# Performance work log

Measured on AMD Instinct MI355X. Metric: run time of the kernel, lower is better.

## Reference

```python
import jax, jax.numpy as jnp
import numpy as np

N_NODES, N_EDGES, N_GRAPHS = 8192, 32768, 256
FXD, HEADS = 78, 10
D2 = FXD * HEADS  # 780
FF = 2048
L_MUT = 735
NF = 32
OUT_DIM = 128


def _ln(x, g, b, eps=1e-5):
    m = x.mean(-1, keepdims=True)
    v = ((x - m) ** 2).mean(-1, keepdims=True)
    return (x - m) * jax.lax.rsqrt(v + eps) * g + b


def _transformer(x, in_w, in_b, out_w, out_b, ln1_g, ln1_b, l1_w, l1_b, l2_w, l2_b, ln2_g, ln2_b):
    # post-LN TransformerEncoderLayer, nhead=1, seq = all N nodes, batch = 1 (eval: dropout off)
    E = x.shape[-1]
    q, k, v = jnp.split(x @ in_w.T + in_b, 3, axis=-1)
    a = jax.nn.softmax((q @ k.T) * (1.0 / np.sqrt(E)), axis=-1) @ v  # [N,N] scores
    x = _ln(x + a @ out_w.T + out_b, ln1_g, ln1_b)
    h = jax.nn.relu(x @ l1_w.T + l1_b) @ l2_w.T + l2_b
    return _ln(x + h, ln2_g, ln2_b)


def _gat(x, src, dst, w, a_src, a_dst, bias):
    # PyG GATConv, heads=10, concat=True, leaky 0.2, self loops already in src/dst
    N = x.shape[0]
    h = (x @ w.T).reshape(N, HEADS, FXD)
    asrc = (h * a_src).sum(-1)  # [N,H]
    adst = (h * a_dst).sum(-1)
    alpha = jax.nn.leaky_relu(asrc[src] + adst[dst], 0.2)  # [E,H]
    amax = jax.lax.stop_gradient(jax.ops.segment_max(alpha, dst, num_segments=N))
    ex = jnp.exp(alpha - amax[dst])
    coef = ex / (jax.ops.segment_sum(ex, dst, num_segments=N)[dst] + 1e-16)
    out = jax.ops.segment_sum(coef[:, :, None] * h[src], dst, num_segments=N)
    return out.reshape(N, HEADS * FXD) + bias


def _gcn(x, src, dst, w, b):
    # PyG GCNConv with self loops (already in src/dst), symmetric norm
    N = x.shape[0]
    deg = jax.ops.segment_sum(jnp.ones(dst.shape, x.dtype), dst, num_segments=N)
    dis = jnp.where(deg > 0, jax.lax.rsqrt(jnp.maximum(deg, 1.0)), 0.0)
    norm = dis[src] * dis[dst]
    return jax.ops.segment_sum(norm[:, None] * (x @ w.T)[src], dst, num_segments=N) + b


def _conv1d(x, w, b):
    y = jax.lax.conv_general_dilated(x, w, (1,), 'VALID', dimension_numbers=('NCH', 'OIH', 'NCH'))
    return y + b[None, :, None]


def _convT1d(x, w, b):
    # torch ConvTranspose1d weight [in,out,k] -> flipped [out,in,k], full padding
    k = w.shape[-1]
    ker = jnp.flip(w, -1).transpose(1, 0, 2)
    y = jax.lax.conv_general_dilated(x, ker, (1,), [(k - 1, k - 1)], dimension_numbers=('NCH', 'OIH', 'NCH'))
    return y + b[None, :, None]


def _maxpool1d(x, k):
    return jax.lax.reduce_window(x, -jnp.inf, jax.lax.max, (1, 1, k), (1, 1, k), 'VALID')


def _bn_eval(x, g, b, eps=1e-5):
    # eval-mode BatchNorm1d with fresh running stats (mean 0, var 1)
    return x * (g / np.sqrt(1.0 + eps))[None, :, None] + b[None, :, None]


def _forward(edge_index, batch, x, target_mut, t1_in_w, t1_in_b, t1_out_w, t1_out_b, t1_ln1_g, t1_ln1_b, t1_l1_w, t1_l1_b, t1_l2_w, t1_l2_b, t1_ln2_g, t1_ln2_b, gat_w, gat_asrc, gat_adst, gat_b, t2_in_w, t2_in_b, t2_out_w, t2_out_b, t2_ln1_g, t2_ln1_b, t2_l1_w, t2_l1_b, t2_l2_w, t2_l2_b, t2_ln2_g, t2_ln2_b, gcn_w, gcn_b, fcg1_w, fcg1_b, fcg2_w, fcg2_b, e1_w, e1_b, bn1_g, bn1_b, e2_w, e2_b, bn2_g, bn2_b, e3_w, e3_b, enc_lin_w, enc_lin_b, d3_w, d3_b, dbn2_g, dbn2_b, d2_w, d2_b, dbn1_g, dbn1_b, d1_w, d1_b, fc1_w, fc1_b, fc2_w, fc2_b, out_w, out_b):
    N = x.shape[0]
    xg = _transformer(x, t1_in_w, t1_in_b, t1_out_w, t1_out_b, t1_ln1_g, t1_ln1_b, t1_l1_w, t1_l1_b, t1_l2_w, t1_l2_b, t1_ln2_g, t1_ln2_b)
    loops = jnp.arange(N, dtype=edge_index.dtype)
    src = jnp.concatenate([edge_index[0], loops])
    dst = jnp.concatenate([edge_index[1], loops])
    xg = jax.nn.relu(_gat(xg, src, dst, gat_w, gat_asrc, gat_adst, gat_b))
    xg = _transformer(xg, t2_in_w, t2_in_b, t2_out_w, t2_out_b, t2_ln1_g, t2_ln1_b, t2_l1_w, t2_l1_b, t2_l2_w, t2_l2_b, t2_ln2_g, t2_ln2_b)
    xg = jax.nn.relu(_gcn(xg, src, dst, gcn_w, gcn_b))
    gm = jax.ops.segment_max(xg, batch, num_segments=N_GRAPHS)
    gm = jnp.where(jnp.isfinite(gm), gm, 0.0)
    cnt = jax.ops.segment_sum(jnp.ones((N,), xg.dtype), batch, num_segments=N_GRAPHS)
    ga = jax.ops.segment_sum(xg, batch, num_segments=N_GRAPHS) / jnp.maximum(cnt, 1.0)[:, None]
    xd = jnp.concatenate([gm, ga], axis=1)  # [B, 1560]
    xd = jax.nn.relu(xd @ fcg1_w.T + fcg1_b)
    xd = xd @ fcg2_w.T + fcg2_b  # [B, 128]
    # conv1d autoencoder on mutation profile
    t = target_mut[:, None, :]  # [B,1,735]
    e = jax.nn.leaky_relu(_bn_eval(_maxpool1d(_conv1d(t, e1_w, e1_b), 8), bn1_g, bn1_b))
    e = jax.nn.leaky_relu(_bn_eval(_maxpool1d(_conv1d(e, e2_w, e2_b), 7), bn2_g, bn2_b))
    e = _conv1d(e, e3_w, e3_b)  # [B,128,5]
    z = e.reshape(e.shape[0], -1) @ enc_lin_w.T + enc_lin_b  # [B,128]
    d = jnp.repeat(jax.nn.leaky_relu(_bn_eval(_convT1d(e, d3_w, d3_b), dbn2_g, dbn2_b)), 7, axis=-1)
    d = jnp.repeat(jax.nn.leaky_relu(_bn_eval(_convT1d(d, d2_w, d2_b), dbn1_g, dbn1_b)), 8, axis=-1)
    decode = _convT1d(d, d1_w, d1_b)  # [B,1,735]
    xc = jnp.concatenate([xd, z], axis=1)
    xc = jax.nn.relu(xc @ fc1_w.T + fc1_b)
    xc = jax.nn.relu(xc @ fc2_w.T + fc2_b)
    out = jax.nn.sigmoid(xc @ out_w.T + out_b)
    return (out, xd, decode)


def setup_inputs():
    key = jax.random.key(0)
    ks = iter(jax.random.split(key, 64))

    def rn(*shape):
        return jax.random.normal(next(ks), shape, jnp.float32) * 0.05

    inp = {}
    inp['x'] = jax.random.normal(next(ks), (N_NODES, FXD), jnp.float32)
    inp['edge_index'] = jax.random.randint(next(ks), (2, N_EDGES), 0, N_NODES)
    inp['batch'] = jnp.sort(jax.random.randint(next(ks), (N_NODES,), 0, N_GRAPHS))
    inp['target_mut'] = jax.random.normal(next(ks), (N_GRAPHS, L_MUT), jnp.float32)
    for p, E in (('t1', FXD), ('t2', D2)):
        inp[p + '_in_w'] = rn(3 * E, E); inp[p + '_in_b'] = jnp.zeros((3 * E,))
        inp[p + '_out_w'] = rn(E, E); inp[p + '_out_b'] = jnp.zeros((E,))
        inp[p + '_ln1_g'] = jnp.ones((E,)); inp[p + '_ln1_b'] = jnp.zeros((E,))
        inp[p + '_l1_w'] = rn(FF, E); inp[p + '_l1_b'] = jnp.zeros((FF,))
        inp[p + '_l2_w'] = rn(E, FF); inp[p + '_l2_b'] = jnp.zeros((E,))
        inp[p + '_ln2_g'] = jnp.ones((E,)); inp[p + '_ln2_b'] = jnp.zeros((E,))
    inp['gat_w'] = rn(D2, FXD); inp['gat_asrc'] = rn(HEADS, FXD); inp['gat_adst'] = rn(HEADS, FXD); inp['gat_b'] = jnp.zeros((D2,))
    inp['gcn_w'] = rn(D2, D2); inp['gcn_b'] = jnp.zeros((D2,))
    inp['fcg1_w'] = rn(1500, 2 * D2); inp['fcg1_b'] = jnp.zeros((1500,))
    inp['fcg2_w'] = rn(OUT_DIM, 1500); inp['fcg2_b'] = jnp.zeros((OUT_DIM,))
    inp['e1_w'] = rn(NF, 1, 8); inp['e1_b'] = jnp.zeros((NF,))
    inp['bn1_g'] = jnp.ones((NF,)); inp['bn1_b'] = jnp.zeros((NF,))
    inp['e2_w'] = rn(2 * NF, NF, 8); inp['e2_b'] = jnp.zeros((2 * NF,))
    inp['bn2_g'] = jnp.ones((2 * NF,)); inp['bn2_b'] = jnp.zeros((2 * NF,))
    inp['e3_w'] = rn(4 * NF, 2 * NF, 8); inp['e3_b'] = jnp.zeros((4 * NF,))
    inp['enc_lin_w'] = rn(OUT_DIM, 640); inp['enc_lin_b'] = jnp.zeros((OUT_DIM,))
    inp['d3_w'] = rn(4 * NF, 2 * NF, 8); inp['d3_b'] = jnp.zeros((2 * NF,))
    inp['dbn2_g'] = jnp.ones((2 * NF,)); inp['dbn2_b'] = jnp.zeros((2 * NF,))
    inp['d2_w'] = rn(2 * NF, NF, 8); inp['d2_b'] = jnp.zeros((NF,))
    inp['dbn1_g'] = jnp.ones((NF,)); inp['dbn1_b'] = jnp.zeros((NF,))
    inp['d1_w'] = rn(NF, 1, 8); inp['d1_b'] = jnp.zeros((1,))
    inp['fc1_w'] = rn(1024, 2 * OUT_DIM); inp['fc1_b'] = jnp.zeros((1024,))
    inp['fc2_w'] = rn(128, 1024); inp['fc2_b'] = jnp.zeros((128,))
    inp['out_w'] = rn(1, 128); inp['out_b'] = jnp.zeros((1,))
    return inp


def reference(x, edge_index, batch, target_mut, t1_in_w, t1_in_b, t1_out_w, t1_out_b, t1_ln1_g, t1_ln1_b, t1_l1_w, t1_l1_b, t1_l2_w, t1_l2_b, t1_ln2_g, t1_ln2_b, gat_w, gat_asrc, gat_adst, gat_b, t2_in_w, t2_in_b, t2_out_w, t2_out_b, t2_ln1_g, t2_ln1_b, t2_l1_w, t2_l1_b, t2_l2_w, t2_l2_b, t2_ln2_g, t2_ln2_b, gcn_w, gcn_b, fcg1_w, fcg1_b, fcg2_w, fcg2_b, e1_w, e1_b, bn1_g, bn1_b, e2_w, e2_b, bn2_g, bn2_b, e3_w, e3_b, enc_lin_w, enc_lin_b, d3_w, d3_b, dbn2_g, dbn2_b, d2_w, d2_b, dbn1_g, dbn1_b, d1_w, d1_b, fc1_w, fc1_b, fc2_w, fc2_b, out_w, out_b):
    return _forward(edge_index, batch, x, target_mut, t1_in_w, t1_in_b, t1_out_w, t1_out_b, t1_ln1_g, t1_ln1_b, t1_l1_w, t1_l1_b, t1_l2_w, t1_l2_b, t1_ln2_g, t1_ln2_b, gat_w, gat_asrc, gat_adst, gat_b, t2_in_w, t2_in_b, t2_out_w, t2_out_b, t2_ln1_g, t2_ln1_b, t2_l1_w, t2_l1_b, t2_l2_w, t2_l2_b, t2_ln2_g, t2_ln2_b, gcn_w, gcn_b, fcg1_w, fcg1_b, fcg2_w, fcg2_b, e1_w, e1_b, bn1_g, bn1_b, e2_w, e2_b, bn2_g, bn2_b, e3_w, e3_b, enc_lin_w, enc_lin_b, d3_w, d3_b, dbn2_g, dbn2_b, d2_w, d2_b, dbn1_g, dbn1_b, d1_w, d1_b, fc1_w, fc1_b, fc2_w, fc2_b, out_w, out_b)
```

## Files before the change

### kernel.cpp

```cpp
#include <hip/hip_runtime.h>
#include <math.h>

#define NN     8192
#define NEDGE  32768
#define NETOT  40960
#define NG     256
#define FXD_   78
#define NH     10
#define DD2    780
#define FFD    2048
#define LMUT   735

static inline int cdiv_i(long long a, int b){ return (int)((a + (long long)b - 1) / b); }
static inline int pad32(int x){ return (x + 31) & ~31; }

typedef __attribute__((ext_vector_type(8))) short bf16x8;
typedef __attribute__((ext_vector_type(4))) float f32x4;

static __device__ __forceinline__ unsigned short f2bf(float f){
    unsigned u = __float_as_uint(f);
    u += 0x7FFFu + ((u >> 16) & 1u);
    return (unsigned short)(u >> 16);
}

static __device__ __forceinline__ void gload16(const void* g, void* l){
    __builtin_amdgcn_global_load_lds((const __attribute__((address_space(1))) void*)g,
                                     (__attribute__((address_space(3))) void*)l, 16, 0, 0);
}

__global__ void fill_f32_k(float* __restrict__ p, float v, long long n){
    long long i = (long long)blockIdx.x * 256 + threadIdx.x;
    if (i < n) p[i] = v;
}
__global__ void fill_u32_k(unsigned* __restrict__ p, unsigned v, long long n){
    long long i = (long long)blockIdx.x * 256 + threadIdx.x;
    if (i < n) p[i] = v;
}

__global__ void cvt_pad_k(const float* __restrict__ src, unsigned short* __restrict__ dst,
                          long long n , int C, int lds_, int ldd)
{
    long long i = (long long)blockIdx.x * 256 + threadIdx.x;
    if (i >= n) return;
    int r = (int)(i / ldd), c = (int)(i % ldd);
    dst[i] = (c < C) ? f2bf(src[(size_t)r * lds_ + c]) : (unsigned short)0;
}

__global__ void tr_bf16_k(const unsigned short* __restrict__ src, unsigned short* __restrict__ dst,
                          int R, int C, int lds_, int ldd)
{
    __shared__ unsigned short t[32][33];
    int cb = blockIdx.x * 32, rb = blockIdx.y * 32;
    int tx = threadIdx.x & 31, ty = threadIdx.x >> 5;
#pragma unroll
    for (int i = 0; i < 4; ++i){
        int r = rb + ty + i * 8, c = cb + tx;
        t[ty + i * 8][tx] = (r < R && c < C) ? src[(size_t)r * lds_ + c] : (unsigned short)0;
    }
    __syncthreads();
#pragma unroll
    for (int i = 0; i < 4; ++i){
        int dr = cb + ty + i * 8, dc = rb + tx;
        if (dr < C && dc < R) dst[(size_t)dr * ldd + dc] = t[tx][ty + i * 8];
    }
}

__global__ void qkv_bias_k(const float* __restrict__ b3, float* __restrict__ out, int E, int Ep)
{
    int idx = blockIdx.x * 256 + threadIdx.x;
    if (idx >= 3 * Ep) return;
    int s = idx / Ep, c = idx % Ep;
    out[idx] = (c < E) ? b3[s * E + c] : 0.f;
}

__global__ void bias_add_k(float* __restrict__ X, const float* __restrict__ b, long long n, int cols)
{
    long long i = (long long)blockIdx.x * 256 + threadIdx.x;
    if (i < n) X[i] += b[i % cols];
}

template<int OUTC, int ACT, int SPLITK, int BROW, int BN>
__global__ __launch_bounds__(256) void mgemm_k(
    const unsigned short* __restrict__ A, const unsigned short* __restrict__ B,
    const float* __restrict__ bias, void* __restrict__ Cv,
    int M, int N, int Kp, int lda, int ldb, int ldc, int swz)
{
    constexpr int NFJ   = BN / 32;
    constexpr int TILEA = 128 * 32;
    constexpr int TILEB = BN * 32;
    __shared__ unsigned short As[2 * TILEA];
    __shared__ unsigned short Bs[2 * TILEB];
    const int tid = threadIdx.x;
    const int lane = tid & 63, wid = tid >> 6;
    const int r16 = lane & 15, q = lane >> 4;
    const int wr = (wid >> 1) * 64, wc = (wid & 1) * (BN / 2);

    const int gx = gridDim.x, gy = gridDim.y;
    const int nwg = gx * gy;
    int orig = swz ? ((int)blockIdx.x * gy + (int)blockIdx.y)
                   : ((int)blockIdx.y * gx + (int)blockIdx.x);
    int q8 = nwg >> 3, r8 = nwg & 7;
    int xcd = orig & 7, kk8 = orig >> 3;
    int wgid = (xcd < r8 ? xcd * (q8 + 1) : r8 * (q8 + 1) + (xcd - r8) * q8) + kk8;
    int bx, by;
    if (swz){ by = wgid % gy; bx = wgid / gy; }
    else    { bx = wgid % gx; by = wgid / gx; }
    const int row0 = by * 128, col0 = bx * BN;

    int kbeg = 0, kend = Kp;
    if (SPLITK > 1){
        int nt_ = Kp >> 5, cpt = (nt_ + SPLITK - 1) / SPLITK;
        kbeg = (int)blockIdx.z * cpt * 32;
        kend = min(Kp, kbeg + cpt * 32);
    }

    const int c0 = wid * 128 + lane;
    const int r0a = c0 >> 2, k0a = (c0 & 3) << 3;
    const size_t gA0 = (size_t)min(row0 + r0a, M - 1) * lda + k0a;
    const size_t gA1 = (size_t)min(row0 + r0a + 16, M - 1) * lda + k0a;
    unsigned short* lA = As + wid * 1024;
    size_t gB0 = 0, gB1 = 0;
    unsigned short* lB;
    if (BN == 128){
        gB0 = (size_t)min(col0 + r0a, N - 1) * ldb + k0a;
        gB1 = (size_t)min(col0 + r0a + 16, N - 1) * ldb + k0a;
        lB = Bs + wid * 1024;
    } else {
        const int cb = wid * 64 + lane;
        const int rb_ = cb >> 2, kb_ = (cb & 3) << 3;
        gB0 = (size_t)min(col0 + rb_, N - 1) * ldb + kb_;
        lB = Bs + wid * 512;
    }

    f32x4 acc[4][NFJ];
#pragma unroll
    for (int i = 0; i < 4; ++i)
#pragma unroll
        for (int j = 0; j < NFJ; ++j){ f32x4 z = {0.f, 0.f, 0.f, 0.f}; acc[i][j] = z; }

    const int nt = (kend - kbeg) >> 5;
    if (nt > 0){
        gload16(A + gA0 + kbeg, lA);
        gload16(A + gA1 + kbeg, lA + 512);
        gload16(B + gB0 + kbeg, lB);
        if (BN == 128) gload16(B + gB1 + kbeg, lB + 512);
        __syncthreads();
        int cur = 0;
        for (int t = 0; t < nt; ++t){
            const int k0 = kbeg + (t << 5);
            if (t + 1 < nt){
                const int kn = k0 + 32, nb = cur ^ 1;
                gload16(A + gA0 + kn, lA + nb * TILEA);
                gload16(A + gA1 + kn, lA + nb * TILEA + 512);
                gload16(B + gB0 + kn, lB + nb * TILEB);
                if (BN == 128) gload16(B + gB1 + kn, lB + nb * TILEB + 512);
            }
            const unsigned short* Ab = As + cur * TILEA;
            const unsigned short* Bb = Bs + cur * TILEB;
            bf16x8 af[4], bfv[NFJ];
#pragma unroll
            for (int f = 0; f < 4; ++f)
                af[f] = *(const bf16x8*)(Ab + (size_t)(wr + f * 16 + r16) * 32 + (q << 3));
#pragma unroll
            for (int f = 0; f < NFJ; ++f)
                bfv[f] = *(const bf16x8*)(Bb + (size_t)(wc + f * 16 + r16) * 32 + (q << 3));
#pragma unroll
            for (int fi = 0; fi < 4; ++fi)
#pragma unroll
                for (int fj = 0; fj < NFJ; ++fj)
                    acc[fi][fj] = __builtin_amdgcn_mfma_f32_16x16x32_bf16(af[fi], bfv[fj], acc[fi][fj], 0, 0, 0);
            __syncthreads();
            cur ^= 1;
        }
    }

#pragma unroll
    for (int fi = 0; fi < 4; ++fi){
#pragma unroll
        for (int j = 0; j < 4; ++j){
            int r = row0 + wr + fi * 16 + q * 4 + j;
            if (r >= M) continue;
#pragma unroll
            for (int fj = 0; fj < NFJ; ++fj){
                int c = col0 + wc + fj * 16 + r16;
                if (c >= N) continue;
                float v = acc[fi][fj][j];
                if (SPLITK > 1){
                    atomicAdd((float*)Cv + (size_t)r * ldc + c, v);
                } else {
                    if (bias) v += BROW ? bias[r] : bias[c];
                    if (ACT == 1) v = fmaxf(v, 0.f);
                    if (ACT == 2) v = 1.f / (1.f + expf(-v));
                    if (OUTC == 0) ((float*)Cv)[(size_t)r * ldc + c] = v;
                    else ((unsigned short*)Cv)[(size_t)r * ldc + c] = f2bf(v);
                }
            }
        }
    }
}

template<int OUTC, int ACT, int SPLITK, int BROW, int BN>
static void mgemm(hipStream_t s, const unsigned short* A, const unsigned short* B,
                  const float* bias, void* C, int M, int N, int Kp,
                  int lda, int ldb, int ldc, int swz)
{
    dim3 g(cdiv_i(N, BN), cdiv_i(M, 128), SPLITK);
    mgemm_k<OUTC, ACT, SPLITK, BROW, BN><<<g, 256, 0, s>>>(A, B, bias, C, M, N, Kp, lda, ldb, ldc, swz);
}

__global__ __launch_bounds__(256) void softmax_bf16_k(unsigned short* __restrict__ SP, float scale)
{
    __shared__ float red[8];
    const int tid = threadIdx.x;
    uint4* prow = (uint4*)(SP + (size_t)blockIdx.x * NN);
    float v[32];
    float mx = -3.4e38f;
#pragma unroll
    for (int c = 0; c < 4; ++c){
        uint4 t = prow[c * 256 + tid];
        const unsigned* u = (const unsigned*)&t;
#pragma unroll
        for (int j = 0; j < 4; ++j){
            float lo = __uint_as_float(u[j] << 16) * scale;
            float hi = __uint_as_float(u[j] & 0xFFFF0000u) * scale;
            v[c * 8 + j * 2]     = lo;
            v[c * 8 + j * 2 + 1] = hi;
            mx = fmaxf(mx, fmaxf(lo, hi));
        }
    }
#pragma unroll
    for (int off = 32; off; off >>= 1) mx = fmaxf(mx, __shfl_xor(mx, off, 64));
    if ((tid & 63) == 0) red[tid >> 6] = mx;
    __syncthreads();
    mx = fmaxf(fmaxf(red[0], red[1]), fmaxf(red[2], red[3]));
    float sum = 0.f;
#pragma unroll
    for (int i = 0; i < 32; ++i){ v[i] = expf(v[i] - mx); sum += v[i]; }
#pragma unroll
    for (int off = 32; off; off >>= 1) sum += __shfl_xor(sum, off, 64);
    if ((tid & 63) == 0) red[4 + (tid >> 6)] = sum;
    __syncthreads();
    float inv = 1.f / (red[4] + red[5] + red[6] + red[7]);
#pragma unroll
    for (int c = 0; c < 4; ++c){
        uint4 t;
        unsigned* u = (unsigned*)&t;
#pragma unroll
        for (int j = 0; j < 4; ++j){
            unsigned lo = f2bf(v[c * 8 + j * 2] * inv);
            unsigned hi = f2bf(v[c * 8 + j * 2 + 1] * inv);
            u[j] = lo | (hi << 16);
        }
        prow[c * 256 + tid] = t;
    }
}

__global__ __launch_bounds__(256) void add_ln_k(
    const float* __restrict__ X, const float* __restrict__ Y, const float* __restrict__ ybias,
    const float* __restrict__ g, const float* __restrict__ b,
    float* __restrict__ out, unsigned short* __restrict__ obf, int E, int Ep)
{
    __shared__ float s1[256], s2[256];
    const int tid = threadIdx.x;
    long long base = (long long)blockIdx.x * E;
    float vals[4];
    float sum = 0.f, sq = 0.f;
    int i = 0;
    for (int c = tid; c < Ep; c += 256, ++i){
        float v = 0.f;
        if (c < E){
            v = X[base + c] + Y[base + c];
            if (ybias) v += ybias[c];
            sum += v; sq += v * v;
        }
        vals[i] = v;
    }
    s1[tid] = sum; s2[tid] = sq; __syncthreads();
    for (int s = 128; s; s >>= 1){
        if (tid < s){ s1[tid] += s1[tid + s]; s2[tid] += s2[tid + s]; }
        __syncthreads();
    }
    float mean = s1[0] / (float)E;
    float var = s2[0] / (float)E - mean * mean;
    if (var < 0.f) var = 0.f;
    float inv = 1.f / sqrtf(var + 1e-5f);
    i = 0;
    for (int c = tid; c < Ep; c += 256, ++i){
        if (c < E){
            float o = (vals[i] - mean) * inv * g[c] + b[c];
            out[base + c] = o;
            if (obf) obf[(size_t)blockIdx.x * Ep + c] = f2bf(o);
        } else if (obf) obf[(size_t)blockIdx.x * Ep + c] = 0;
    }
}

static __device__ __forceinline__ unsigned enc_f(float x){
    unsigned u = __float_as_uint(x);
    return (u & 0x80000000u) ? ~u : (u | 0x80000000u);
}
static __device__ __forceinline__ float dec_f(unsigned u){
    return (u & 0x80000000u) ? __uint_as_float(u & 0x7fffffffu) : __uint_as_float(~u);
}
static __device__ __forceinline__ void edge_sd(const int* __restrict__ ei, int e, int& s, int& d){
    if (e < NEDGE){ s = ei[e]; d = ei[NEDGE + e]; }
    else { s = e - NEDGE; d = e - NEDGE; }
}

__global__ void gat_srcdst_k(const float* __restrict__ h, const float* __restrict__ aw_src,
                             const float* __restrict__ aw_dst, float* __restrict__ asrc,
                             float* __restrict__ adst)
{
    int idx = blockIdx.x * 256 + threadIdx.x;
    if (idx >= NN * NH) return;
    int n = idx / NH, hh = idx % NH;
    const float* hp = h + (long long)n * DD2 + hh * FXD_;
    const float* ws = aw_src + hh * FXD_;
    const float* wd = aw_dst + hh * FXD_;
    float s1 = 0.f, s2 = 0.f;
    for (int f = 0; f < FXD_; ++f){ float v = hp[f]; s1 += v * ws[f]; s2 += v * wd[f]; }
    asrc[idx] = s1; adst[idx] = s2;
}

__global__ void gat_alpha_k(const int* __restrict__ ei, const float* __restrict__ asrc,
                            const float* __restrict__ adst, float* __restrict__ alpha,
                            unsigned* __restrict__ amax)
{
    int idx = blockIdx.x * 256 + threadIdx.x;
    if (idx >= NETOT * NH) return;
    int e = idx / NH, hh = idx % NH;
    int s, d; edge_sd(ei, e, s, d);
    float a = asrc[s * NH + hh] + adst[d * NH + hh];
    a = (a > 0.f) ? a : 0.2f * a;
    alpha[idx] = a;
    atomicMax(&amax[d * NH + hh], enc_f(a));
}

__global__ void gat_expsum_k(const int* __restrict__ ei, float* __restrict__ alpha,
                             const unsigned* __restrict__ amax, float* __restrict__ denom)
{
    int idx = blockIdx.x * 256 + threadIdx.x;
    if (idx >= NETOT * NH) return;
    int e = idx / NH, hh = idx % NH;
    int s, d; edge_sd(ei, e, s, d);
    float m = dec_f(amax[d * NH + hh]);
    float ex = expf(alpha[idx] - m);
    alpha[idx] = ex;
    atomicAdd(&denom[d * NH + hh], ex);
}

__global__ void deg_count_k(const int* __restrict__ ei, int* __restrict__ deg)
{
    int e = blockIdx.x * 256 + threadIdx.x;
    if (e >= NETOT) return;
    int s, d; edge_sd(ei, e, s, d);
    atomicAdd(&deg[d], 1);
}

__global__ __launch_bounds__(256) void csr_off_k(const int* __restrict__ deg,
                                                 int* __restrict__ off, int* __restrict__ cur)
{
    __shared__ int pref[257];
    const int tid = threadIdx.x;
    int loc[32];
    int base = tid * 32, sum = 0;
#pragma unroll
    for (int i = 0; i < 32; ++i){ loc[i] = sum; sum += deg[base + i]; }
    __shared__ int part[256];
    part[tid] = sum; __syncthreads();
    if (tid == 0){
        pref[0] = 0;
        for (int i = 0; i < 256; ++i) pref[i + 1] = pref[i] + part[i];
    }
    __syncthreads();
    int p0 = pref[tid];
#pragma unroll
    for (int i = 0; i < 32; ++i){ off[base + i] = p0 + loc[i]; cur[base + i] = p0 + loc[i]; }
    if (tid == 0) off[NN] = pref[256];
}

__global__ void csr_fill_k(const int* __restrict__ ei, int* __restrict__ cur,
                           int* __restrict__ csr_s, int* __restrict__ csr_e)
{
    int e = blockIdx.x * 256 + threadIdx.x;
    if (e >= NETOT) return;
    int s, d; edge_sd(ei, e, s, d);
    int pos = atomicAdd(&cur[d], 1);
    csr_s[pos] = s; csr_e[pos] = e;
}

__global__ __launch_bounds__(256) void gat_gather_k(
    const int* __restrict__ off, const int* __restrict__ csr_s, const int* __restrict__ csr_e,
    const float* __restrict__ ex, const float* __restrict__ denom,
    const float* __restrict__ hfeat, float* __restrict__ out)
{
    const int d = blockIdx.x, tid = threadIdx.x;
    const int beg = off[d], end = off[d + 1];
    for (int f = tid; f < DD2; f += 256){
        int hh = f / FXD_;
        float acc = 0.f;
        for (int p = beg; p < end; ++p)
            acc += ex[csr_e[p] * NH + hh] * hfeat[(size_t)csr_s[p] * DD2 + f];
        out[(size_t)d * DD2 + f] = acc / (denom[d * NH + hh] + 1e-16f);
    }
}

__global__ __launch_bounds__(256) void gcn_gather_k(
    const int* __restrict__ off, const int* __restrict__ csr_s,
    const float* __restrict__ dis, const float* __restrict__ xw, float* __restrict__ out)
{
    const int d = blockIdx.x, tid = threadIdx.x;
    const int beg = off[d], end = off[d + 1];
    const float dd_ = dis[d];
    for (int f = tid; f < DD2; f += 256){
        float acc = 0.f;
        for (int p = beg; p < end; ++p){
            int s = csr_s[p];
            acc += dis[s] * xw[(size_t)s * DD2 + f];
        }
        out[(size_t)d * DD2 + f] = acc * dd_;
    }
}

__global__ void bias_relu_k(float* __restrict__ X, const float* __restrict__ b,
                            unsigned short* __restrict__ obf, int rows, int cols, int ldp)
{
    long long i = (long long)blockIdx.x * 256 + threadIdx.x;
    if (i >= (long long)rows * ldp) return;
    int r = (int)(i / ldp), c = (int)(i % ldp);
    if (c < cols){
        float v = X[(size_t)r * cols + c] + b[c];
        v = v > 0.f ? v : 0.f;
        X[(size_t)r * cols + c] = v;
        if (obf) obf[i] = f2bf(v);
    } else if (obf) obf[i] = 0;
}

__global__ void dis_k(const int* __restrict__ deg, float* __restrict__ dis)
{
    int n = blockIdx.x * 256 + threadIdx.x;
    if (n >= NN) return;
    float d = (float)deg[n];
    dis[n] = (d > 0.f) ? 1.f / sqrtf(fmaxf(d, 1.f)) : 0.f;
}

__global__ void pool_accum_k(const float* __restrict__ xg, const int* __restrict__ batch,
                             float* __restrict__ gm, float* __restrict__ ga, int* __restrict__ cnt)
{
    long long idx = (long long)blockIdx.x * 256 + threadIdx.x;
    if (idx >= (long long)NN * DD2) return;
    int n = (int)(idx / DD2), f = (int)(idx % DD2);
    int g = batch[n];
    float v = xg[idx];
    atomicMax((int*)(gm + (long long)g * DD2 + f), __float_as_int(v));
    atomicAdd(ga + (long long)g * DD2 + f, v);
    if (f == 0) atomicAdd(cnt + g, 1);
}

__global__ void pool_fin_k(const float* __restrict__ gm, const float* __restrict__ ga,
                           const int* __restrict__ cnt, unsigned short* __restrict__ xdb)
{
    int idx = blockIdx.x * 256 + threadIdx.x;
    if (idx >= NG * 1568) return;
    int g = idx / 1568, c = idx % 1568;
    float v = 0.f;
    if (c < DD2)       v = gm[g * DD2 + c];
    else if (c < 1560) v = ga[g * DD2 + (c - DD2)] / fmaxf((float)cnt[g], 1.f);
    xdb[idx] = f2bf(v);
}

#define BN_SCALE 0.9999950000374996f

__global__ __launch_bounds__(256) void enc1_b(const float* __restrict__ tm, const float* __restrict__ w,
                                              const float* __restrict__ bias, const float* __restrict__ bng,
                                              const float* __restrict__ bnb, float* __restrict__ out)
{
    __shared__ float xs[736];
    __shared__ float ws[256], bs[32], gs[32], b2[32];
    const int g = blockIdx.x, tid = threadIdx.x;
    for (int i = tid; i < 735; i += 256) xs[i] = tm[(size_t)g * LMUT + i];
    ws[tid] = w[tid];
    if (tid < 32){ bs[tid] = bias[tid]; gs[tid] = bng[tid]; b2[tid] = bnb[tid]; }
    __syncthreads();
    for (int idx = tid; idx < 32 * 91; idx += 256){
        int o = idx / 91, t = idx % 91;
        float mx = -3.4e38f;
        for (int p = 0; p < 8; ++p){
            float s = bs[o];
#pragma unroll
            for (int k = 0; k < 8; ++k) s += xs[t * 8 + p + k] * ws[o * 8 + k];
            mx = fmaxf(mx, s);
        }
        float v = mx * gs[o] * BN_SCALE + b2[o];
        out[(size_t)g * 2912 + idx] = v > 0.f ? v : 0.01f * v;
    }
}

__global__ void i2c_enc2_k(const float* __restrict__ in, unsigned short* __restrict__ A){
    int idx = blockIdx.x * 256 + threadIdx.x;
    if (idx >= NG * 84 * 256) return;
    int col = idx & 255, row = idx >> 8;
    int g = row / 84, u = row % 84;
    int i = col >> 3, k = col & 7;
    A[idx] = f2bf(in[(size_t)g * 2912 + i * 91 + u + k]);
}
__global__ void post_enc2_k(const float* __restrict__ G, const float* __restrict__ b,
                            const float* __restrict__ bng, const float* __restrict__ bnb,
                            float* __restrict__ out){
    int idx = blockIdx.x * 256 + threadIdx.x;
    if (idx >= NG * 768) return;
    int t = idx % 12, o = (idx / 12) & 63, g = idx / 768;
    float mx = -3.4e38f;
#pragma unroll
    for (int p = 0; p < 7; ++p) mx = fmaxf(mx, G[(size_t)(g * 84 + t * 7 + p) * 64 + o]);
    float v = (mx + b[o]) * bng[o] * BN_SCALE + bnb[o];
    out[(size_t)g * 768 + o * 12 + t] = v > 0.f ? v : 0.01f * v;
}
__global__ void i2c_enc3_k(const float* __restrict__ in, unsigned short* __restrict__ A){
    int idx = blockIdx.x * 256 + threadIdx.x;
    if (idx >= NG * 5 * 512) return;
    int col = idx & 511, row = idx >> 9;
    int g = row / 5, t = row % 5;
    int i2 = col >> 3, k = col & 7;
    A[idx] = f2bf(in[(size_t)g * 768 + i2 * 12 + t + k]);
}
__global__ void post_enc3_k(const float* __restrict__ G, const float* __restrict__ b,
                            float* __restrict__ e3o, unsigned short* __restrict__ obf){
    int idx = blockIdx.x * 256 + threadIdx.x;
    if (idx >= NG * 640) return;
    int t = idx % 5, o = (idx / 5) & 127, g = idx / 640;
    float v = G[(size_t)(g * 5 + t) * 128 + o] + b[o];
    e3o[(size_t)g * 640 + o * 5 + t] = v;
    obf[(size_t)g * 640 + o * 5 + t] = f2bf(v);
}
__global__ void wshuf_k(const float* __restrict__ src, unsigned short* __restrict__ dst, int I, int O){
    int idx = blockIdx.x * 256 + threadIdx.x;
    if (idx >= I * O * 8) return;
    int o = idx / (I * 8), rem = idx % (I * 8);
    int i = rem >> 3, j = rem & 7;
    dst[idx] = f2bf(src[(size_t)(i * O + o) * 8 + j]);
}
__global__ void i2c_dec3_k(const float* __restrict__ e3o, unsigned short* __restrict__ A){
    int idx = blockIdx.x * 256 + threadIdx.x;
    if (idx >= NG * 12 * 1024) return;
    int col = idx & 1023, row = idx >> 10;
    int g = row / 12, t = row % 12;
    int i2 = col >> 3, j = col & 7;
    int tt = t - j;
    A[idx] = (tt >= 0 && tt < 5) ? f2bf(e3o[(size_t)g * 640 + i2 * 5 + tt]) : (unsigned short)0;
}
__global__ void post_dec3_k(const float* __restrict__ G, const float* __restrict__ b,
                            const float* __restrict__ bng, const float* __restrict__ bnb,
                            float* __restrict__ dd3){
    int idx = blockIdx.x * 256 + threadIdx.x;
    if (idx >= NG * 768) return;
    int t = idx % 12, o = (idx / 12) & 63, g = idx / 768;
    float v = (G[(size_t)(g * 12 + t) * 64 + o] + b[o]) * bng[o] * BN_SCALE + bnb[o];
    dd3[(size_t)g * 768 + o * 12 + t] = v > 0.f ? v : 0.01f * v;
}
__global__ void i2c_dec2_k(const float* __restrict__ dd3, unsigned short* __restrict__ A){
    int idx = blockIdx.x * 256 + threadIdx.x;
    if (idx >= NG * 91 * 512) return;
    int col = idx & 511, row = idx >> 9;
    int g = row / 91, t = row % 91;
    int i2 = col >> 3, j = col & 7;
    int tt = t - j;
    A[idx] = (tt >= 0 && tt < 84) ? f2bf(dd3[(size_t)g * 768 + i2 * 12 + tt / 7]) : (unsigned short)0;
}
__global__ void post_dec2_k(const float* __restrict__ G, const float* __restrict__ b,
                            const float* __restrict__ bng, const float* __restrict__ bnb,
                            float* __restrict__ dd2){
    int idx = blockIdx.x * 256 + threadIdx.x;
    if (idx >= NG * 2912) return;
    int t = idx % 91, o = (idx / 91) & 31, g = idx / 2912;
    float v = (G[(size_t)(g * 91 + t) * 32 + o] + b[o]) * bng[o] * BN_SCALE + bnb[o];
    dd2[(size_t)g * 2912 + o * 91 + t] = v > 0.f ? v : 0.01f * v;
}

__global__ __launch_bounds__(256) void dec1_b(const float* __restrict__ dd2, const float* __restrict__ w,
                                              const float* __restrict__ bias, float* __restrict__ out)
{
    __shared__ float d2s[32][91];
    __shared__ float ws[256];
    const int g = blockIdx.x, tid = threadIdx.x;
    const int t0 = (int)blockIdx.y * 245;
    for (int i = tid; i < 32 * 91; i += 256) d2s[i / 91][i % 91] = dd2[(size_t)g * 2912 + i];
    ws[tid] = w[tid];
    __syncthreads();
    if (tid < 245){
        int t = t0 + tid;
        int id8[8]; bool ok[8];
#pragma unroll
        for (int j = 0; j < 8; ++j){
            int tt = t - j;
            ok[j] = (tt >= 0 && tt < 728);
            id8[j] = ok[j] ? (tt >> 3) : 0;
        }
        float s = bias[0];
        for (int i2 = 0; i2 < 32; ++i2){
            const float* wp = ws + i2 * 8;
            float a = 0.f;
#pragma unroll
            for (int j = 0; j < 8; ++j) if (ok[j]) a += d2s[i2][id8[j]] * wp[j];
            s += a;
        }
        out[(size_t)g * 735 + t] = s;
    }
}

__global__ void concat_xc_k(const float* __restrict__ xd, const float* __restrict__ z,
                            unsigned short* __restrict__ xcb)
{
    int idx = blockIdx.x * 256 + threadIdx.x;
    if (idx >= NG * 256) return;
    int g = idx >> 8, c = idx & 255;
    xcb[idx] = f2bf((c < 128) ? xd[g * 128 + c] : z[g * 128 + (c - 128)]);
}

extern "C" void kernel_launch(void* const* d_in, const int* in_sizes, int n_in,
                              void* d_out, int out_size, void* d_ws, size_t ws_size,
                              hipStream_t stream)
{
    (void)in_sizes; (void)n_in; (void)out_size;

    const float* x      = (const float*)d_in[0];
    const int*   ei     = (const int*)  d_in[1];
    const int*   batch  = (const int*)  d_in[2];
    const float* tmut   = (const float*)d_in[3];
    const float* t1w[12]; for (int i = 0; i < 12; ++i) t1w[i] = (const float*)d_in[4 + i];
    const float* t2w[12]; for (int i = 0; i < 12; ++i) t2w[i] = (const float*)d_in[16 + i];
    const float* gat_w    = (const float*)d_in[28];
    const float* gat_asrc = (const float*)d_in[29];
    const float* gat_adst = (const float*)d_in[30];
    const float* gat_b    = (const float*)d_in[31];
    const float* gcn_w  = (const float*)d_in[32];
    const float* gcn_b  = (const float*)d_in[33];
    const float* fcg1_w = (const float*)d_in[34];
    const float* fcg1_b = (const float*)d_in[35];
    const float* fcg2_w = (const float*)d_in[36];
    const float* fcg2_b = (const float*)d_in[37];
    const float* e1_w = (const float*)d_in[38]; const float* e1_b = (const float*)d_in[39];
    const float* bn1_g = (const float*)d_in[40]; const float* bn1_b = (const float*)d_in[41];
    const float* e2_w = (const float*)d_in[42]; const float* e2_b = (const float*)d_in[43];
    const float* bn2_g = (const float*)d_in[44]; const float* bn2_b = (const float*)d_in[45];
    const float* e3_w = (const float*)d_in[46]; const float* e3_b = (const float*)d_in[47];
    const float* enc_w = (const float*)d_in[48]; const float* enc_b = (const float*)d_in[49];
    const float* d3_w = (const float*)d_in[50]; const float* d3_b = (const float*)d_in[51];
    const float* dbn2_g = (const float*)d_in[52]; const float* dbn2_b = (const float*)d_in[53];
    const float* d2_w = (const float*)d_in[54]; const float* d2_b = (const float*)d_in[55];
    const float* dbn1_g = (const float*)d_in[56]; const float* dbn1_b = (const float*)d_in[57];
    const float* d1_w = (const float*)d_in[58]; const float* d1_b = (const float*)d_in[59];
    const float* fc1_w = (const float*)d_in[60]; const float* fc1_b = (const float*)d_in[61];
    const float* fc2_w = (const float*)d_in[62]; const float* fc2_b = (const float*)d_in[63];
    const float* outw = (const float*)d_in[64]; const float* outb = (const float*)d_in[65];

    float *A1, *A2, *A3, *A4, *X1f, *QBIASf;
    unsigned short *XB, *QKVb, *Vt, *HbPb;
    unsigned short *WQKVb, *WOUTb, *WL1b, *WL2b, *WGb, *WGCNb, *WFCG1b, *WFCG2b,
                   *WENCb, *WFC1b, *WFC2b, *WOUTWb, *XD16, *FG1b, *E3b, *XCb, *FH1b, *FH2b, *Wcvb;
    float *asrc, *adst, *alpha, *denom, *dis, *gm, *ga, *c1p, *c2p, *e3o,
          *zz, *dd3, *dd2b;
    unsigned *amax; int *deg, *cnt, *csr_off, *csr_cur, *csr_s, *csr_e;

    auto carve = [&](long long RB) -> size_t {
        char* wp_ = (char*)d_ws;
        auto alc = [&](size_t bytes) -> char* {
            char* p = wp_;
            wp_ += (bytes + 255) & ~(size_t)255;
            return p;
        };
        A1 = (float*)alc((size_t)NN * DD2 * 4);
        A2 = (float*)alc((size_t)NN * DD2 * 4);
        A3 = (float*)alc((size_t)NN * DD2 * 4);
        A4 = (float*)alc((size_t)NN * DD2 * 4);
        X1f = (float*)alc((size_t)NN * FXD_ * 4);
        XB   = (unsigned short*)alc((size_t)NN * 800 * 2);
        QKVb = (unsigned short*)alc((size_t)NN * 2400 * 2);
        Vt   = (unsigned short*)alc((size_t)800 * NN * 2);
        size_t hb = (size_t)NN * FFD * 2, pb = (size_t)RB * NN * 2;
        HbPb = (unsigned short*)alc(hb > pb ? hb : pb);
        WQKVb = (unsigned short*)alc((size_t)2400 * 800 * 2);
        QBIASf= (float*)alc((size_t)2400 * 4);
        WOUTb = (unsigned short*)alc((size_t)780 * 800 * 2);
        WL1b  = (unsigned short*)alc((size_t)2048 * 800 * 2);
        WL2b  = (unsigned short*)alc((size_t)780 * 2048 * 2);
        WGb   = (unsigned short*)alc((size_t)780 * 96 * 2);
        WGCNb = (unsigned short*)alc((size_t)780 * 800 * 2);
        WFCG1b= (unsigned short*)alc((size_t)1500 * 1568 * 2);
        WFCG2b= (unsigned short*)alc((size_t)128 * 1504 * 2);
        WENCb = (unsigned short*)alc((size_t)128 * 640 * 2);
        WFC1b = (unsigned short*)alc((size_t)1024 * 256 * 2);
        WFC2b = (unsigned short*)alc((size_t)128 * 1024 * 2);
        WOUTWb= (unsigned short*)alc((size_t)128 * 2);
        Wcvb  = (unsigned short*)alc((size_t)128 * 1024 * 2);
        XD16  = (unsigned short*)alc((size_t)NG * 1568 * 2);
        FG1b  = (unsigned short*)alc((size_t)NG * 1504 * 2);
        E3b   = (unsigned short*)alc((size_t)NG * 640 * 2);
        XCb   = (unsigned short*)alc((size_t)NG * 256 * 2);
        FH1b  = (unsigned short*)alc((size_t)NG * 1024 * 2);
        FH2b  = (unsigned short*)alc((size_t)NG * 128 * 2);
        asrc = (float*)alc((size_t)NN * NH * 4);
        adst = (float*)alc((size_t)NN * NH * 4);
        alpha= (float*)alc((size_t)NETOT * NH * 4);
        amax = (unsigned*)alc((size_t)NN * NH * 4);
        denom= (float*)alc((size_t)NN * NH * 4);
        deg  = (int*)alc((size_t)NN * 4);
        dis  = (float*)alc((size_t)NN * 4);
        cnt  = (int*)alc((size_t)NG * 4);
        csr_off = (int*)alc((size_t)(NN + 1) * 4);
        csr_cur = (int*)alc((size_t)NN * 4);
        csr_s   = (int*)alc((size_t)NETOT * 4);
        csr_e   = (int*)alc((size_t)NETOT * 4);
        gm   = (float*)alc((size_t)NG * DD2 * 4);
        ga   = (float*)alc((size_t)NG * DD2 * 4);
        c1p  = (float*)alc((size_t)NG * 32 * 91 * 4);
        c2p  = (float*)alc((size_t)NG * 64 * 12 * 4);
        e3o  = (float*)alc((size_t)NG * 128 * 5 * 4);
        zz   = (float*)alc((size_t)NG * 128 * 4);
        dd3  = (float*)alc((size_t)NG * 64 * 12 * 4);
        dd2b = (float*)alc((size_t)NG * 32 * 91 * 4);
        return (size_t)(wp_ - (char*)d_ws);
    };

    long long RB = 512;
    const long long cands[5] = {8192, 4096, 2048, 1024, 512};
    for (int i = 0; i < 5; ++i){ if (carve(cands[i]) <= ws_size){ RB = cands[i]; break; } }
    carve(RB);
    unsigned short* Pb = HbPb;
    unsigned short* AIM = HbPb;

    float* out0   = (float*)d_out;
    float* xd_out = (float*)d_out + NG;
    float* decode = (float*)d_out + NG + NG * 128;

    auto cvt = [&](const float* src, unsigned short* dst, int R, int C, int lds_, int ldd){
        long long n = (long long)R * ldd;
        cvt_pad_k<<<cdiv_i(n, 256), 256, 0, stream>>>(src, dst, n, C, lds_, ldd);
    };
    auto zero16 = [&](unsigned short* p, long long nshorts){
        fill_u32_k<<<cdiv_i(nshorts / 2, 256), 256, 0, stream>>>((unsigned*)p, 0u, nshorts / 2);
    };
    auto zerof = [&](float* p, long long n){
        fill_f32_k<<<cdiv_i(n, 256), 256, 0, stream>>>(p, 0.f, n);
    };

    auto run_tf = [&](const float* xin, const float* const* W, float* outp, int E){
        const int Ep = pad32(E), E3p = 3 * Ep;
        float scale = (float)(1.0 / sqrt((double)E));
        zero16(WQKVb, (long long)E3p * Ep);
        for (int s = 0; s < 3; ++s)
            cvt(W[0] + (size_t)s * E * E, WQKVb + (size_t)s * Ep * Ep, E, E, E, Ep);
        qkv_bias_k<<<cdiv_i(E3p, 256), 256, 0, stream>>>(W[1], QBIASf, E, Ep);
        mgemm<1,0,1,0,128>(stream, XB, WQKVb, QBIASf, QKVb, NN, E3p, Ep, Ep, Ep, E3p, 0);
        {
            dim3 g(cdiv_i(E, 32), cdiv_i(NN, 32));
            tr_bf16_k<<<g, 256, 0, stream>>>(QKVb + 2 * Ep, Vt, NN, E, E3p, NN);
        }
        zerof(A4, (long long)NN * E);
        for (long long r0 = 0; r0 < NN; r0 += RB){
            mgemm<1,0,1,0,128>(stream, QKVb + (size_t)r0 * E3p, QKVb + Ep, nullptr, Pb,
                               (int)RB, NN, Ep, E3p, E3p, NN, 0);
            softmax_bf16_k<<<(int)RB, 256, 0, stream>>>(Pb, scale);
            if (E == FXD_)
                mgemm<0,0,8,0,64>(stream, Pb, Vt, nullptr, A4 + (size_t)r0 * E,
                                  (int)RB, E, NN, NN, NN, E, 0);
            else
                mgemm<0,0,4,0,64>(stream, Pb, Vt, nullptr, A4 + (size_t)r0 * E,
                                  (int)RB, E, NN, NN, NN, E, 0);
        }
        cvt(A4, XB, NN, E, E, Ep);
        cvt(W[2], WOUTb, E, E, E, Ep);
        mgemm<0,0,1,0,64>(stream, XB, WOUTb, W[3], A2, NN, E, Ep, Ep, Ep, E, 0);
        add_ln_k<<<NN, 256, 0, stream>>>(xin, A2, nullptr, W[4], W[5], A3, XB, E, Ep);
        cvt(W[6], WL1b, FFD, E, E, Ep);
        mgemm<1,1,1,0,128>(stream, XB, WL1b, W[7], HbPb, NN, FFD, Ep, Ep, Ep, FFD, 0);
        cvt(W[8], WL2b, E, FFD, FFD, FFD);
        mgemm<0,0,1,0,64>(stream, HbPb, WL2b, W[9], A2, NN, E, FFD, FFD, FFD, E, 0);
        add_ln_k<<<NN, 256, 0, stream>>>(A3, A2, nullptr, W[10], W[11], outp, XB, E, Ep);
    };

    cvt(x, XB, NN, FXD_, FXD_, 96);
    run_tf(x, t1w, X1f, FXD_);

    fill_u32_k<<<cdiv_i(NN, 256), 256, 0, stream>>>((unsigned*)deg, 0u, NN);
    deg_count_k<<<cdiv_i(NETOT, 256), 256, 0, stream>>>(ei, deg);
    csr_off_k<<<1, 256, 0, stream>>>(deg, csr_off, csr_cur);
    csr_fill_k<<<cdiv_i(NETOT, 256), 256, 0, stream>>>(ei, csr_cur, csr_s, csr_e);

    cvt(gat_w, WGb, DD2, FXD_, FXD_, 96);
    mgemm<0,0,1,0,64>(stream, XB, WGb, nullptr, A2, NN, DD2, 96, 96, 96, DD2, 0);
    gat_srcdst_k<<<cdiv_i((long long)NN * NH, 256), 256, 0, stream>>>(A2, gat_asrc, gat_adst, asrc, adst);
    fill_u32_k<<<cdiv_i((long long)NN * NH, 256), 256, 0, stream>>>(amax, 0x007FFFFFu, (long long)NN * NH);
    zerof(denom, (long long)NN * NH);
    gat_alpha_k<<<cdiv_i((long long)NETOT * NH, 256), 256, 0, stream>>>(ei, asrc, adst, alpha, amax);
    gat_expsum_k<<<cdiv_i((long long)NETOT * NH, 256), 256, 0, stream>>>(ei, alpha, amax, denom);
    gat_gather_k<<<NN, 256, 0, stream>>>(csr_off, csr_s, csr_e, alpha, denom, A2, A1);
    bias_relu_k<<<cdiv_i((long long)NN * 800, 256), 256, 0, stream>>>(A1, gat_b, XB, NN, DD2, 800);

    run_tf(A1, t2w, A1, DD2);

    dis_k<<<cdiv_i(NN, 256), 256, 0, stream>>>(deg, dis);
    cvt(gcn_w, WGCNb, DD2, DD2, DD2, 800);
    mgemm<0,0,1,0,64>(stream, XB, WGCNb, nullptr, A2, NN, DD2, 800, 800, 800, DD2, 0);
    gcn_gather_k<<<NN, 256, 0, stream>>>(csr_off, csr_s, dis, A2, A3);
    bias_relu_k<<<cdiv_i((long long)NN * DD2, 256), 256, 0, stream>>>(A3, gcn_b, nullptr, NN, DD2, DD2);

    zerof(gm, (long long)NG * DD2);
    zerof(ga, (long long)NG * DD2);
    fill_u32_k<<<cdiv_i(NG, 256), 256, 0, stream>>>((unsigned*)cnt, 0u, NG);
    pool_accum_k<<<cdiv_i((long long)NN * DD2, 256), 256, 0, stream>>>(A3, batch, gm, ga, cnt);
    pool_fin_k<<<cdiv_i((long long)NG * 1568, 256), 256, 0, stream>>>(gm, ga, cnt, XD16);
    cvt(fcg1_w, WFCG1b, 1500, 1560, 1560, 1568);
    zerof(A2, (long long)NG * 1500);
    mgemm<0,0,8,0,64>(stream, XD16, WFCG1b, nullptr, A2, NG, 1500, 1568, 1568, 1568, 1500, 0);
    bias_relu_k<<<cdiv_i((long long)NG * 1504, 256), 256, 0, stream>>>(A2, fcg1_b, FG1b, NG, 1500, 1504);
    cvt(fcg2_w, WFCG2b, 128, 1500, 1500, 1504);
    zerof(xd_out, (long long)NG * 128);
    mgemm<0,0,16,0,128>(stream, FG1b, WFCG2b, nullptr, xd_out, NG, 128, 1504, 1504, 1504, 128, 0);
    bias_add_k<<<cdiv_i((long long)NG * 128, 256), 256, 0, stream>>>(xd_out, fcg2_b, (long long)NG * 128, 128);

    enc1_b<<<NG, 256, 0, stream>>>(tmut, e1_w, e1_b, bn1_g, bn1_b, c1p);
    i2c_enc2_k<<<cdiv_i((long long)NG * 84 * 256, 256), 256, 0, stream>>>(c1p, AIM);
    cvt(e2_w, Wcvb, 64, 256, 256, 256);
    mgemm<0,0,1,0,64>(stream, AIM, Wcvb, nullptr, A2, NG * 84, 64, 256, 256, 256, 64, 0);
    post_enc2_k<<<cdiv_i((long long)NG * 768, 256), 256, 0, stream>>>(A2, e2_b, bn2_g, bn2_b, c2p);
    i2c_enc3_k<<<cdiv_i((long long)NG * 5 * 512, 256), 256, 0, stream>>>(c2p, AIM);
    cvt(e3_w, Wcvb, 128, 512, 512, 512);
    zerof(A2, (long long)NG * 5 * 128);
    mgemm<0,0,4,0,128>(stream, AIM, Wcvb, nullptr, A2, NG * 5, 128, 512, 512, 512, 128, 0);
    post_enc3_k<<<cdiv_i((long long)NG * 640, 256), 256, 0, stream>>>(A2, e3_b, e3o, E3b);
    cvt(enc_w, WENCb, 128, 640, 640, 640);
    mgemm<0,0,1,0,128>(stream, E3b, WENCb, enc_b, zz, NG, 128, 640, 640, 640, 128, 0);

    wshuf_k<<<cdiv_i(128 * 64 * 8, 256), 256, 0, stream>>>(d3_w, Wcvb, 128, 64);
    i2c_dec3_k<<<cdiv_i((long long)NG * 12 * 1024, 256), 256, 0, stream>>>(e3o, AIM);
    zerof(A2, (long long)NG * 12 * 64);
    mgemm<0,0,4,0,64>(stream, AIM, Wcvb, nullptr, A2, NG * 12, 64, 1024, 1024, 1024, 64, 0);
    post_dec3_k<<<cdiv_i((long long)NG * 768, 256), 256, 0, stream>>>(A2, d3_b, dbn2_g, dbn2_b, dd3);
    wshuf_k<<<cdiv_i(64 * 32 * 8, 256), 256, 0, stream>>>(d2_w, Wcvb, 64, 32);
    i2c_dec2_k<<<cdiv_i((long long)NG * 91 * 512, 256), 256, 0, stream>>>(dd3, AIM);
    mgemm<0,0,1,0,64>(stream, AIM, Wcvb, nullptr, A2, NG * 91, 32, 512, 512, 512, 32, 0);
    post_dec2_k<<<cdiv_i((long long)NG * 2912, 256), 256, 0, stream>>>(A2, d2_b, dbn1_g, dbn1_b, dd2b);
    { dim3 g(NG, 3); dec1_b<<<g, 256, 0, stream>>>(dd2b, d1_w, d1_b, decode); }

    concat_xc_k<<<cdiv_i((long long)NG * 256, 256), 256, 0, stream>>>(xd_out, zz, XCb);
    cvt(fc1_w, WFC1b, 1024, 256, 256, 256);
    mgemm<1,1,1,0,128>(stream, XCb, WFC1b, fc1_b, FH1b, NG, 1024, 256, 256, 256, 1024, 0);
    cvt(fc2_w, WFC2b, 128, 1024, 1024, 1024);
    zerof(A3, (long long)NG * 128);
    mgemm<0,0,8,0,128>(stream, FH1b, WFC2b, nullptr, A3, NG, 128, 1024, 1024, 1024, 128, 0);
    bias_relu_k<<<cdiv_i((long long)NG * 128, 256), 256, 0, stream>>>(A3, fc2_b, FH2b, NG, 128, 128);
    cvt(outw, WOUTWb, 1, 128, 128, 128);
    mgemm<0,2,1,0,64>(stream, FH2b, WOUTWb, outb, out0, NG, 1, 128, 128, 128, 1, 0);
}
```

Measured before the change: 1.787 ms.

## Replace atomic graph pooling with segment-based pooling and cap attention row block

Global max/mean pooling over graphs now uses per-graph node ranges computed from the sorted batch vector, with one block per graph reducing its rows directly. This removes float atomics, the zero-init and the finalize kernels. The attention row-block candidates are capped at 2048, and the QK^T GEMM gets a different trailing flag. Max initialised at 0 relies on the inputs being post-ReLU and batch being sorted.

```diff
diff --git a/kernel.cpp b/kernel.cpp
--- a/kernel.cpp
+++ b/kernel.cpp
@@ -443,29 +443,35 @@
     dis[n] = (d > 0.f) ? 1.f / sqrtf(fmaxf(d, 1.f)) : 0.f;
 }
 
-__global__ void pool_accum_k(const float* __restrict__ xg, const int* __restrict__ batch,
-                             float* __restrict__ gm, float* __restrict__ ga, int* __restrict__ cnt)
-{
-    long long idx = (long long)blockIdx.x * 256 + threadIdx.x;
-    if (idx >= (long long)NN * DD2) return;
-    int n = (int)(idx / DD2), f = (int)(idx % DD2);
-    int g = batch[n];
-    float v = xg[idx];
-    atomicMax((int*)(gm + (long long)g * DD2 + f), __float_as_int(v));
-    atomicAdd(ga + (long long)g * DD2 + f, v);
-    if (f == 0) atomicAdd(cnt + g, 1);
-}
-
-__global__ void pool_fin_k(const float* __restrict__ gm, const float* __restrict__ ga,
-                           const int* __restrict__ cnt, unsigned short* __restrict__ xdb)
-{
-    int idx = blockIdx.x * 256 + threadIdx.x;
-    if (idx >= NG * 1568) return;
-    int g = idx / 1568, c = idx % 1568;
-    float v = 0.f;
-    if (c < DD2)       v = gm[g * DD2 + c];
-    else if (c < 1560) v = ga[g * DD2 + (c - DD2)] / fmaxf((float)cnt[g], 1.f);
-    xdb[idx] = f2bf(v);
+__global__ void seg_start_k(const int* __restrict__ batch, int* __restrict__ start)
+{
+    int n = blockIdx.x * 256 + threadIdx.x;
+    if (n >= NN) return;
+    int b = batch[n];
+    int bp = (n == 0) ? -1 : batch[n - 1];
+    for (int g = bp + 1; g <= b; ++g) start[g] = n;
+    if (n == NN - 1){
+        for (int g = b + 1; g <= NG; ++g) start[g] = NN;
+    }
+}
+
+__global__ __launch_bounds__(256) void pool_seg_k(const float* __restrict__ xg,
+                                                  const int* __restrict__ start,
+                                                  unsigned short* __restrict__ xdb)
+{
+    const int g = blockIdx.x, tid = threadIdx.x;
+    const int s0 = start[g], s1 = start[g + 1];
+    const float inv = 1.f / fmaxf((float)(s1 - s0), 1.f);
+    for (int f = tid; f < DD2; f += 256){
+        float mx = 0.f, sm = 0.f;
+        for (int n = s0; n < s1; ++n){
+            float v = xg[(size_t)n * DD2 + f];
+            mx = fmaxf(mx, v); sm += v;
+        }
+        xdb[(size_t)g * 1568 + f] = f2bf(mx);
+        xdb[(size_t)g * 1568 + DD2 + f] = f2bf(sm * inv);
+    }
+    if (tid < 8) xdb[(size_t)g * 1568 + 1560 + tid] = 0;
 }
 
 #define BN_SCALE 0.9999950000374996f
@@ -657,9 +663,8 @@
     unsigned short *XB, *QKVb, *Vt, *HbPb;
     unsigned short *WQKVb, *WOUTb, *WL1b, *WL2b, *WGb, *WGCNb, *WFCG1b, *WFCG2b,
                    *WENCb, *WFC1b, *WFC2b, *WOUTWb, *XD16, *FG1b, *E3b, *XCb, *FH1b, *FH2b, *Wcvb;
-    float *asrc, *adst, *alpha, *denom, *dis, *gm, *ga, *c1p, *c2p, *e3o,
-          *zz, *dd3, *dd2b;
-    unsigned *amax; int *deg, *cnt, *csr_off, *csr_cur, *csr_s, *csr_e;
+    float *asrc, *adst, *alpha, *denom, *dis, *c1p, *c2p, *e3o, *zz, *dd3, *dd2b;
+    unsigned *amax; int *deg, *seg, *csr_off, *csr_cur, *csr_s, *csr_e;
 
     auto carve = [&](long long RB) -> size_t {
         char* wp_ = (char*)d_ws;
@@ -705,13 +710,11 @@
         denom= (float*)alc((size_t)NN * NH * 4);
         deg  = (int*)alc((size_t)NN * 4);
         dis  = (float*)alc((size_t)NN * 4);
-        cnt  = (int*)alc((size_t)NG * 4);
+        seg  = (int*)alc((size_t)(NG + 1) * 4);
         csr_off = (int*)alc((size_t)(NN + 1) * 4);
         csr_cur = (int*)alc((size_t)NN * 4);
         csr_s   = (int*)alc((size_t)NETOT * 4);
         csr_e   = (int*)alc((size_t)NETOT * 4);
-        gm   = (float*)alc((size_t)NG * DD2 * 4);
-        ga   = (float*)alc((size_t)NG * DD2 * 4);
         c1p  = (float*)alc((size_t)NG * 32 * 91 * 4);
         c2p  = (float*)alc((size_t)NG * 64 * 12 * 4);
         e3o  = (float*)alc((size_t)NG * 128 * 5 * 4);
@@ -722,8 +725,8 @@
     };
 
     long long RB = 512;
-    const long long cands[5] = {8192, 4096, 2048, 1024, 512};
-    for (int i = 0; i < 5; ++i){ if (carve(cands[i]) <= ws_size){ RB = cands[i]; break; } }
+    const long long cands[3] = {2048, 1024, 512};
+    for (int i = 0; i < 3; ++i){ if (carve(cands[i]) <= ws_size){ RB = cands[i]; break; } }
     carve(RB);
     unsigned short* Pb = HbPb;
     unsigned short* AIM = HbPb;
@@ -758,7 +761,7 @@
         zerof(A4, (long long)NN * E);
         for (long long r0 = 0; r0 < NN; r0 += RB){
             mgemm<1,0,1,0,128>(stream, QKVb + (size_t)r0 * E3p, QKVb + Ep, nullptr, Pb,
-                               (int)RB, NN, Ep, E3p, E3p, NN, 0);
+                               (int)RB, NN, Ep, E3p, E3p, NN, 1);
             softmax_bf16_k<<<(int)RB, 256, 0, stream>>>(Pb, scale);
             if (E == FXD_)
                 mgemm<0,0,8,0,64>(stream, Pb, Vt, nullptr, A4 + (size_t)r0 * E,
@@ -785,6 +788,7 @@
     deg_count_k<<<cdiv_i(NETOT, 256), 256, 0, stream>>>(ei, deg);
     csr_off_k<<<1, 256, 0, stream>>>(deg, csr_off, csr_cur);
     csr_fill_k<<<cdiv_i(NETOT, 256), 256, 0, stream>>>(ei, csr_cur, csr_s, csr_e);
+    seg_start_k<<<cdiv_i(NN, 256), 256, 0, stream>>>(batch, seg);
 
     cvt(gat_w, WGb, DD2, FXD_, FXD_, 96);
     mgemm<0,0,1,0,64>(stream, XB, WGb, nullptr, A2, NN, DD2, 96, 96, 96, DD2, 0);
@@ -804,11 +808,7 @@
     gcn_gather_k<<<NN, 256, 0, stream>>>(csr_off, csr_s, dis, A2, A3);
     bias_relu_k<<<cdiv_i((long long)NN * DD2, 256), 256, 0, stream>>>(A3, gcn_b, nullptr, NN, DD2, DD2);
 
-    zerof(gm, (long long)NG * DD2);
-    zerof(ga, (long long)NG * DD2);
-    fill_u32_k<<<cdiv_i(NG, 256), 256, 0, stream>>>((unsigned*)cnt, 0u, NG);
-    pool_accum_k<<<cdiv_i((long long)NN * DD2, 256), 256, 0, stream>>>(A3, batch, gm, ga, cnt);
-    pool_fin_k<<<cdiv_i((long long)NG * 1568, 256), 256, 0, stream>>>(gm, ga, cnt, XD16);
+    pool_seg_k<<<NG, 256, 0, stream>>>(A3, seg, XD16);
     cvt(fcg1_w, WFCG1b, 1500, 1560, 1560, 1568);
     zerof(A2, (long long)NG * 1500);
     mgemm<0,0,8,0,64>(stream, XD16, WFCG1b, nullptr, A2, NG, 1500, 1568, 1568, 1568, 1500, 0);
```

Result: no change. 1.766 ms (-1.2%).
